# Optimization experiments

Hardware: AMD Instinct MI355X
Metric: run time of the kernel (lower is better)

## Reference

```python
import jax, jax.numpy as jnp
import numpy as np

SHAPES = ((28, 28, 28), (14, 14, 14), (7, 7, 7))  # (D,H,W) per level, hardcoded by offset_normalizer
M, L, P = 6, 3, 4  # n_heads, n_levels, n_points


def grid_sample_3d(vol, grid):
    """Trilinear grid sample, zeros padding, align_corners=False.
    vol: (B, C, D, H, W); grid: (B, Q, 3) with xyz in [-1,1] (x->W, y->H, z->D).
    Returns (B, C, Q)."""
    B, C, D, H, W = vol.shape
    x = ((grid[..., 0] + 1.0) * W - 1.0) * 0.5
    y = ((grid[..., 1] + 1.0) * H - 1.0) * 0.5
    z = ((grid[..., 2] + 1.0) * D - 1.0) * 0.5
    x0f = jnp.floor(x); y0f = jnp.floor(y); z0f = jnp.floor(z)
    fx = x - x0f; fy = y - y0f; fz = z - z0f
    x0 = x0f.astype(jnp.int32); y0 = y0f.astype(jnp.int32); z0 = z0f.astype(jnp.int32)
    flat = vol.reshape(B, C, D * H * W)
    out = jnp.zeros((B, C, grid.shape[1]), vol.dtype)
    for dz, wz in ((0, 1.0 - fz), (1, fz)):
        for dy, wy in ((0, 1.0 - fy), (1, fy)):
            for dx, wx in ((0, 1.0 - fx), (1, fx)):
                zi = z0 + dz; yi = y0 + dy; xi = x0 + dx
                valid = (zi >= 0) & (zi < D) & (yi >= 0) & (yi < H) & (xi >= 0) & (xi < W)
                idx = (jnp.clip(zi, 0, D - 1) * H + jnp.clip(yi, 0, H - 1)) * W + jnp.clip(xi, 0, W - 1)
                g = jnp.take_along_axis(flat, idx[:, None, :], axis=2)  # (B,C,Q)
                w = (wz * wy * wx) * valid.astype(vol.dtype)
                out = out + g * w[:, None, :]
    return out


def setup_inputs() -> dict:
    key = jax.random.key(0)
    ks = jax.random.split(key, 8)
    bs, Lq, d_model, image_dim, T = 1, 4096, 768, 1408, 2
    S = sum(d * h * w for d, h, w in SHAPES)  # 25039
    return {
        "query": jax.random.normal(ks[0], (bs, Lq, d_model), jnp.float32),
        "reference_points": jax.random.uniform(ks[1], (bs, Lq, 3), jnp.float32),
        "value": jax.random.normal(ks[2], (bs, T, S, image_dim), jnp.float32),
        "Wv": jax.random.normal(ks[3], (image_dim, d_model), jnp.float32) * 0.02,
        "bv": jnp.zeros((d_model,), jnp.float32),
        "Woff": jax.random.normal(ks[4], (d_model, M * T * L * P * 3), jnp.float32) * 0.02,
        "boff": jax.random.normal(ks[5], (M * T * L * P * 3,), jnp.float32) * 0.5,
        "Wa": jax.random.normal(ks[6], (d_model, M * T * L * P), jnp.float32) * 0.02,
        "ba": jnp.zeros((M * T * L * P,), jnp.float32),
        "Wo": jax.random.normal(ks[7], (d_model, d_model), jnp.float32) * 0.02,
        "bo": jnp.zeros((d_model,), jnp.float32),
    }


def reference(query, reference_points, value, Wv, bv, Woff, boff, Wa, ba, Wo, bo):
    N, Lq, d_model = query.shape
    T = value.shape[1]
    Dh = d_model // M
    # value projection + head split: (N,T,S,M,Dh)
    v = (value @ Wv + bv).reshape(N, T, -1, M, Dh)
    # sampling offsets and attention weights from query
    off = (query @ Woff + boff).reshape(N, Lq, M, T, L, P, 3)
    aw = jax.nn.softmax((query @ Wa + ba).reshape(N, Lq, M, T * L * P), axis=-1)
    aw = aw.reshape(N, Lq, M, T, L, P)
    normalizer = jnp.asarray([[28., 28., 28.], [14., 14., 14.], [7., 7., 7.]], query.dtype)
    loc = reference_points[:, :, None, None, None, None, :] + off / normalizer[None, None, None, None, :, None, :]
    grids = 2.0 * loc - 1.0  # (N,Lq,M,T,L,P,3)
    starts = [0]
    for (d, h, w) in SHAPES:
        starts.append(starts[-1] + d * h * w)
    sampled = []
    for l, (Dl, Hl, Wl) in enumerate(SHAPES):
        vl = v[:, :, starts[l]:starts[l + 1]]                       # (N,T,Sl,M,Dh)
        vl = vl.transpose(0, 1, 3, 4, 2).reshape(N * T * M, Dh, Dl, Hl, Wl)
        gl = grids[:, :, :, :, l].transpose(0, 3, 2, 1, 4, 5).reshape(N * T * M, Lq * P, 3)
        sampled.append(grid_sample_3d(vl, gl).reshape(N, T, M, Dh, Lq, P))
    s = jnp.stack(sampled, axis=5)                                  # (N,T,M,Dh,Lq,L,P)
    out = jnp.einsum('ntmdqlp,nqmtlp->nqmd', s, aw).reshape(N, Lq, M * Dh)
    return out @ Wo + bo
```

## Files before the change

### kernel.cpp

```cpp
#include <hip/hip_runtime.h>
#include <hip/hip_bf16.h>
#include <stdint.h>

#define LQ    4096
#define DMOD  768
#define IMGD  1408
#define TT    2
#define MM    6
#define LL    3
#define PP    4
#define DH    128
#define STOT  25039
#define OFFC  432
#define AWC   144
#define PROJC 576
#define NSAMP 24
#define NCORN 192

typedef __attribute__((ext_vector_type(8))) __bf16 bf16x8;
typedef __attribute__((ext_vector_type(4))) float  f32x4;

__device__ __forceinline__ void gl_lds16(const void* g, void* l) {
    __builtin_amdgcn_global_load_lds(
        (const __attribute__((address_space(1))) void*)g,
        (__attribute__((address_space(3))) void*)l, 16, 0, 0);
}

__global__ __launch_bounds__(256) void cvt_transpose(
    const float* __restrict__ W, __bf16* __restrict__ WT, int K, int N)
{
    __shared__ float tile[32][33];
    const int k0 = blockIdx.x * 32, n0 = blockIdx.y * 32;
    const int c = threadIdx.x & 31, r8 = threadIdx.x >> 5;
    #pragma unroll
    for (int i = 0; i < 4; ++i) {
        int r = r8 + i * 8;
        int k = k0 + r, n = n0 + c;
        tile[r][c] = (k < K && n < N) ? W[(size_t)k * N + n] : 0.f;
    }
    __syncthreads();
    #pragma unroll
    for (int i = 0; i < 4; ++i) {
        int r = r8 + i * 8;
        int n = n0 + r, k = k0 + c;
        if (n < N && k < K) WT[(size_t)n * K + k] = (__bf16)tile[c][r];
    }
}

__global__ __launch_bounds__(256) void cvt_value(
    const float4* __restrict__ src, __bf16* __restrict__ dst, int n4)
{
    int i = blockIdx.x * blockDim.x + threadIdx.x;
    const int stride = gridDim.x * blockDim.x;
    for (; i < n4; i += stride) {
        float4 v = src[i];
        union { __bf16 h[4]; uint64_t u; } pk;
        pk.h[0] = (__bf16)v.x; pk.h[1] = (__bf16)v.y;
        pk.h[2] = (__bf16)v.z; pk.h[3] = (__bf16)v.w;
        *(uint64_t*)(dst + (size_t)i * 4) = pk.u;
    }
}

__global__ void concat_bias(const float* __restrict__ boff,
                            const float* __restrict__ ba,
                            float* __restrict__ bcat)
{
    int i = blockIdx.x * blockDim.x + threadIdx.x;
    if (i < PROJC) bcat[i] = (i < OFFC) ? boff[i] : ba[i - OFFC];
}

template<bool A_BF16, bool OUT_BF16>
__global__ __launch_bounds__(256) void gemm_mfma(
    const void* __restrict__ Ap, const __bf16* __restrict__ BT,
    const float* __restrict__ bias, void* __restrict__ Cp,
    int M, int N, int K)
{
    __shared__ __bf16 As[128][32];
    __shared__ __bf16 Bs[128][32];

    const int tid  = threadIdx.x;
    const int lane = tid & 63;
    const int wave = tid >> 6;
    const int wm = (wave & 1) * 64;
    const int wn = (wave >> 1) * 64;
    const int row0 = blockIdx.y * 128;
    const int col0 = blockIdx.x * 128;
    const int fr = lane & 15;
    const int kq = lane >> 4;

    const int sr  = tid >> 1;
    const int kk0 = (tid & 1) * 16;

    f32x4 acc[4][4] = {};

    for (int kt = 0; kt < K; kt += 32) {
        #pragma unroll
        for (int j = 0; j < 2; ++j) {
            const int g   = wave * 128 + j * 64 + lane;
            const int row = g >> 2, cir = g & 3;
            const __bf16* src = BT + (size_t)(col0 + row) * K + kt + cir * 8;
            gl_lds16(src, (char*)&Bs[0][0] + (size_t)(wave * 128 + j * 64) * 16);
        }
        if constexpr (A_BF16) {
            const __bf16* A = (const __bf16*)Ap;
            #pragma unroll
            for (int j = 0; j < 2; ++j) {
                const int g   = wave * 128 + j * 64 + lane;
                const int row = g >> 2, cir = g & 3;
                const __bf16* src = A + (size_t)(row0 + row) * K + kt + cir * 8;
                gl_lds16(src, (char*)&As[0][0] + (size_t)(wave * 128 + j * 64) * 16);
            }
        } else {
            const float* A = (const float*)Ap;
            const int gm = row0 + sr;
            float f[16];
            if (gm < M) {
                const float4* ap = (const float4*)(A + (size_t)gm * K + kt + kk0);
                #pragma unroll
                for (int i = 0; i < 4; ++i) {
                    float4 v = ap[i];
                    f[i*4+0] = v.x; f[i*4+1] = v.y; f[i*4+2] = v.z; f[i*4+3] = v.w;
                }
            } else {
                #pragma unroll
                for (int i = 0; i < 16; ++i) f[i] = 0.f;
            }
            bf16x8 v0, v1;
            #pragma unroll
            for (int i = 0; i < 8; ++i) { v0[i] = (__bf16)f[i]; v1[i] = (__bf16)f[i+8]; }
            *(bf16x8*)&As[sr][kk0]     = v0;
            *(bf16x8*)&As[sr][kk0 + 8] = v1;
        }
        __syncthreads();

        bf16x8 a[4], b[4];
        #pragma unroll
        for (int mt = 0; mt < 4; ++mt) a[mt] = *(const bf16x8*)&As[wm + mt*16 + fr][kq * 8];
        #pragma unroll
        for (int nt = 0; nt < 4; ++nt) b[nt] = *(const bf16x8*)&Bs[wn + nt*16 + fr][kq * 8];
        #pragma unroll
        for (int mt = 0; mt < 4; ++mt)
            #pragma unroll
            for (int nt = 0; nt < 4; ++nt)
                acc[mt][nt] = __builtin_amdgcn_mfma_f32_16x16x32_bf16(
                    a[mt], b[nt], acc[mt][nt], 0, 0, 0);
        __syncthreads();
    }

    const int col = lane & 15;
    const int rq  = (lane >> 4) * 4;
    #pragma unroll
    for (int mt = 0; mt < 4; ++mt) {
        #pragma unroll
        for (int r = 0; r < 4; ++r) {
            const int gm = row0 + wm + mt*16 + rq + r;
            if (gm >= M) continue;
            #pragma unroll
            for (int nt = 0; nt < 4; ++nt) {
                const int gn = col0 + wn + nt*16 + col;
                if (gn < N) {
                    float v = acc[mt][nt][r] + bias[gn];
                    if constexpr (OUT_BF16)
                        ((__bf16*)Cp)[(size_t)gm * N + gn] = (__bf16)v;
                    else
                        ((float*)Cp)[(size_t)gm * N + gn] = v;
                }
            }
        }
    }
}

__global__ __launch_bounds__(256) void sample_kernel(
    const float* __restrict__ refp,
    const float* __restrict__ proj,
    const __bf16* __restrict__ vbuf,
    __bf16* __restrict__ attn)
{
    const int wave = threadIdx.x >> 6;
    const int lane = threadIdx.x & 63;
    const int q = blockIdx.x * 4 + wave;
    const int m = blockIdx.y;

    __shared__ float    s_aw[4][NSAMP];
    __shared__ float    s_w[4][NCORN];
    __shared__ uint32_t s_o[4][NCORN];

    if (lane < NSAMP)
        s_aw[wave][lane] = proj[(size_t)q * PROJC + OFFC + m * NSAMP + lane];
    __syncthreads();

    if (lane < NSAMP) {
        float mx = -1e30f;
        #pragma unroll
        for (int i = 0; i < NSAMP; ++i) mx = fmaxf(mx, s_aw[wave][i]);
        float sum = 0.f;
        #pragma unroll
        for (int i = 0; i < NSAMP; ++i) sum += __expf(s_aw[wave][i] - mx);
        const float aww = __expf(s_aw[wave][lane] - mx) / sum;

        const int t = lane / 12;
        const int r = lane - t * 12;
        const int l = r >> 2;
        const int   Dl    = (l == 0) ? 28 : (l == 1) ? 14 : 7;
        const int   start = (l == 0) ? 0  : (l == 1) ? 21952 : 24696;
        const float fD    = (float)Dl;
        const int   base  = t * STOT + start;

        const float* op = proj + (size_t)q * PROJC + m * 72 + lane * 3;
        const float rx = refp[q*3+0], ry = refp[q*3+1], rz = refp[q*3+2];
        float x = rx * fD + op[0] - 0.5f;
        float y = ry * fD + op[1] - 0.5f;
        float z = rz * fD + op[2] - 0.5f;
        float xf = floorf(x), yf = floorf(y), zf = floorf(z);
        float fx = x - xf, fy = y - yf, fz = z - zf;
        int x0 = (int)xf, y0 = (int)yf, z0 = (int)zf;
        float wx[2] = {1.f - fx, fx}, wy[2] = {1.f - fy, fy}, wz[2] = {1.f - fz, fz};
        #pragma unroll
        for (int cc = 0; cc < 8; ++cc) {
            int dx = cc & 1, dy = (cc >> 1) & 1, dz = cc >> 2;
            int xi = x0 + dx, yi = y0 + dy, zi = z0 + dz;
            bool ok = (xi >= 0) & (xi < Dl) & (yi >= 0) & (yi < Dl) &
                      (zi >= 0) & (zi < Dl);
            float    w   = ok ? aww * wx[dx] * wy[dy] * wz[dz] : 0.f;
            uint32_t off = ok ? (uint32_t)(base + (zi * Dl + yi) * Dl + xi) * (768u * 2u) : 0u;
            s_w[wave][lane * 8 + cc] = w;
            s_o[wave][lane * 8 + cc] = off;
        }
    }
    __syncthreads();

    const char* vb = (const char*)vbuf + ((size_t)m * 128 + lane * 2) * 2;
    float acc0 = 0.f, acc1 = 0.f;
    #pragma unroll 8
    for (int i = 0; i < NCORN; ++i) {
        const float    w   = s_w[wave][i];
        const uint32_t off = s_o[wave][i];
        const uint32_t u = *(const uint32_t*)(vb + off);
        acc0 += w * __uint_as_float(u << 16);
        acc1 += w * __uint_as_float(u & 0xffff0000u);
    }

    union { __bf16 h[2]; uint32_t u; } pk;
    pk.h[0] = (__bf16)acc0; pk.h[1] = (__bf16)acc1;
    *(uint32_t*)((char*)attn + ((size_t)q * DMOD + m * 128 + lane * 2) * 2) = pk.u;
}

extern "C" void kernel_launch(void* const* d_in, const int* in_sizes, int n_in,
                              void* d_out, int out_size, void* d_ws, size_t ws_size,
                              hipStream_t stream) {
    const float* query = (const float*)d_in[0];
    const float* refp  = (const float*)d_in[1];
    const float* value = (const float*)d_in[2];
    const float* Wv    = (const float*)d_in[3];
    const float* bv    = (const float*)d_in[4];
    const float* Woff  = (const float*)d_in[5];
    const float* boff  = (const float*)d_in[6];
    const float* Wa    = (const float*)d_in[7];
    const float* ba    = (const float*)d_in[8];
    const float* Wo    = (const float*)d_in[9];
    const float* bo    = (const float*)d_in[10];
    float* out = (float*)d_out;

    const size_t SZ_VALBF = (size_t)TT * STOT * IMGD * 2;
    const size_t SZ_VBUF  = (size_t)TT * STOT * DMOD * 2;
    const size_t SZ_PROJ  = (size_t)LQ * PROJC * 4;
    const size_t SZ_ATTN  = (size_t)LQ * DMOD * 2;
    const size_t SZ_WVT   = (size_t)IMGD * DMOD * 2;
    const size_t SZ_WCAT  = (size_t)PROJC * DMOD * 2;
    const size_t SZ_WOT   = (size_t)DMOD * DMOD * 2;
    const size_t NEED_FAST = SZ_VALBF + SZ_VBUF + SZ_PROJ + SZ_ATTN +
                             SZ_WVT + SZ_WCAT + SZ_WOT + 8192;
    const bool fast = ws_size >= NEED_FAST;

    char* p = (char*)d_ws;
    __bf16* valbf = nullptr;
    if (fast) { valbf = (__bf16*)p; p += SZ_VALBF; }
    __bf16* vbuf  = (__bf16*)p; p += SZ_VBUF;
    float*  proj  = (float*)p;  p += SZ_PROJ;
    __bf16* attn  = (__bf16*)p; p += SZ_ATTN;
    __bf16* wvt   = (__bf16*)p; p += SZ_WVT;
    __bf16* wcatT = (__bf16*)p; p += SZ_WCAT;
    __bf16* woT   = (__bf16*)p; p += SZ_WOT;
    float*  bcat  = (float*)p;

    cvt_transpose<<<dim3((IMGD+31)/32, (DMOD+31)/32), 256, 0, stream>>>(Wv, wvt, IMGD, DMOD);
    cvt_transpose<<<dim3((DMOD+31)/32, (OFFC+31)/32), 256, 0, stream>>>(Woff, wcatT, DMOD, OFFC);
    cvt_transpose<<<dim3((DMOD+31)/32, (AWC +31)/32), 256, 0, stream>>>(Wa, wcatT + (size_t)OFFC * DMOD, DMOD, AWC);
    cvt_transpose<<<dim3((DMOD+31)/32, (DMOD+31)/32), 256, 0, stream>>>(Wo, woT, DMOD, DMOD);
    concat_bias<<<dim3(3), 256, 0, stream>>>(boff, ba, bcat);

    const int Mv = TT * STOT;

    if (fast) {
        cvt_value<<<dim3(4096), 256, 0, stream>>>((const float4*)value, valbf,
                                                  (int)((size_t)TT * STOT * IMGD / 4));
        gemm_mfma<true, true><<<dim3(DMOD/128, (Mv+127)/128), 256, 0, stream>>>(
            valbf, wvt, bv, vbuf, Mv, DMOD, IMGD);
    } else {
        gemm_mfma<false, true><<<dim3(DMOD/128, (Mv+127)/128), 256, 0, stream>>>(
            value, wvt, bv, vbuf, Mv, DMOD, IMGD);
    }

    gemm_mfma<false, false><<<dim3((PROJC+127)/128, LQ/128), 256, 0, stream>>>(
        query, wcatT, bcat, proj, LQ, PROJC, DMOD);

    sample_kernel<<<dim3(LQ/4, MM), 256, 0, stream>>>(refp, proj, vbuf, attn);

    gemm_mfma<true, false><<<dim3(DMOD/128, LQ/128), 256, 0, stream>>>(
        attn, woT, bo, out, LQ, DMOD, DMOD);
}
```

Before: 766.1 us.

## Double-buffer GEMM, fuse value fp32 conversion, swizzle blocks per XCD, widen sampling loads

Drops the separate fp32-to-bf16 conversion pass over the value tensor. The value projection GEMM now reads fp32 directly and converts while staging into LDS. The GEMM gains double-buffered LDS with register prefetch of the next A tile, a single barrier per k-step, occupancy hint 3, and an XCD-aware block-index swizzle for the large value GEMM. The sampling kernel splits corners across wave halves, loads 8 bytes per lane and combines the halves with a cross-lane shuffle. This trades the extra conversion pass for more register pressure and fp32 global reads inside the GEMM.

```diff
diff --git a/kernel.cpp b/kernel.cpp
--- a/kernel.cpp
+++ b/kernel.cpp
@@ -47,20 +47,6 @@
     }
 }
 
-__global__ __launch_bounds__(256) void cvt_value(
-    const float4* __restrict__ src, __bf16* __restrict__ dst, int n4)
-{
-    int i = blockIdx.x * blockDim.x + threadIdx.x;
-    const int stride = gridDim.x * blockDim.x;
-    for (; i < n4; i += stride) {
-        float4 v = src[i];
-        union { __bf16 h[4]; uint64_t u; } pk;
-        pk.h[0] = (__bf16)v.x; pk.h[1] = (__bf16)v.y;
-        pk.h[2] = (__bf16)v.z; pk.h[3] = (__bf16)v.w;
-        *(uint64_t*)(dst + (size_t)i * 4) = pk.u;
-    }
-}
-
 __global__ void concat_bias(const float* __restrict__ boff,
                             const float* __restrict__ ba,
                             float* __restrict__ bcat)
@@ -69,82 +55,119 @@
     if (i < PROJC) bcat[i] = (i < OFFC) ? boff[i] : ba[i - OFFC];
 }
 
-template<bool A_BF16, bool OUT_BF16>
-__global__ __launch_bounds__(256) void gemm_mfma(
+template<int AF32, int OUT_BF16, int SWZ>
+__global__ __launch_bounds__(256, 3) void gemm_mfma(
     const void* __restrict__ Ap, const __bf16* __restrict__ BT,
     const float* __restrict__ bias, void* __restrict__ Cp,
     int M, int N, int K)
 {
-    __shared__ __bf16 As[128][32];
-    __shared__ __bf16 Bs[128][32];
+    __shared__ __bf16 As[2][128][32];
+    __shared__ __bf16 Bs[2][128][32];
 
     const int tid  = threadIdx.x;
     const int lane = tid & 63;
     const int wave = tid >> 6;
     const int wm = (wave & 1) * 64;
     const int wn = (wave >> 1) * 64;
-    const int row0 = blockIdx.y * 128;
-    const int col0 = blockIdx.x * 128;
+
+    int bx, by;
+    if constexpr (SWZ > 0) {
+        const int bid = blockIdx.x;
+        const int xcd = bid & 7;
+        const int slot = bid >> 3;
+        const int ppx = (gridDim.x >> 3) / SWZ;
+        const int pix = slot / SWZ;
+        bx = slot - pix * SWZ;
+        by = xcd * ppx + pix;
+    } else {
+        bx = blockIdx.x; by = blockIdx.y;
+    }
+    const int row0 = by * 128;
+    const int col0 = bx * 128;
+
     const int fr = lane & 15;
     const int kq = lane >> 4;
 
     const int sr  = tid >> 1;
     const int kk0 = (tid & 1) * 16;
-
-    f32x4 acc[4][4] = {};
-
-    for (int kt = 0; kt < K; kt += 32) {
+    const int gB_row = (wave * 128 + lane) >> 2;
+    (void)gB_row;
+
+    float f[16];
+
+    auto stageB = [&](int ki, int buf) {
         #pragma unroll
         for (int j = 0; j < 2; ++j) {
             const int g   = wave * 128 + j * 64 + lane;
             const int row = g >> 2, cir = g & 3;
-            const __bf16* src = BT + (size_t)(col0 + row) * K + kt + cir * 8;
-            gl_lds16(src, (char*)&Bs[0][0] + (size_t)(wave * 128 + j * 64) * 16);
-        }
-        if constexpr (A_BF16) {
-            const __bf16* A = (const __bf16*)Ap;
+            const __bf16* src = BT + (size_t)(col0 + row) * K + ki * 32 + cir * 8;
+            gl_lds16(src, (char*)&Bs[buf][0][0] + (size_t)(wave * 128 + j * 64) * 16);
+        }
+    };
+    auto stageA_lds = [&](int ki, int buf) {
+        const __bf16* A = (const __bf16*)Ap;
+        #pragma unroll
+        for (int j = 0; j < 2; ++j) {
+            const int g   = wave * 128 + j * 64 + lane;
+            const int row = g >> 2, cir = g & 3;
+            const __bf16* src = A + (size_t)(row0 + row) * K + ki * 32 + cir * 8;
+            gl_lds16(src, (char*)&As[buf][0][0] + (size_t)(wave * 128 + j * 64) * 16);
+        }
+    };
+    auto loadA_f32 = [&](int ki) {
+        const float* A = (const float*)Ap;
+        const int gm = row0 + sr;
+        if (gm < M) {
+            const float4* ap = (const float4*)(A + (size_t)gm * K + ki * 32 + kk0);
             #pragma unroll
-            for (int j = 0; j < 2; ++j) {
-                const int g   = wave * 128 + j * 64 + lane;
-                const int row = g >> 2, cir = g & 3;
-                const __bf16* src = A + (size_t)(row0 + row) * K + kt + cir * 8;
-                gl_lds16(src, (char*)&As[0][0] + (size_t)(wave * 128 + j * 64) * 16);
+            for (int i = 0; i < 4; ++i) {
+                float4 v = ap[i];
+                f[i*4+0] = v.x; f[i*4+1] = v.y; f[i*4+2] = v.z; f[i*4+3] = v.w;
             }
         } else {
-            const float* A = (const float*)Ap;
-            const int gm = row0 + sr;
-            float f[16];
-            if (gm < M) {
-                const float4* ap = (const float4*)(A + (size_t)gm * K + kt + kk0);
-                #pragma unroll
-                for (int i = 0; i < 4; ++i) {
-                    float4 v = ap[i];
-                    f[i*4+0] = v.x; f[i*4+1] = v.y; f[i*4+2] = v.z; f[i*4+3] = v.w;
-                }
-            } else {
-                #pragma unroll
-                for (int i = 0; i < 16; ++i) f[i] = 0.f;
-            }
-            bf16x8 v0, v1;
             #pragma unroll
-            for (int i = 0; i < 8; ++i) { v0[i] = (__bf16)f[i]; v1[i] = (__bf16)f[i+8]; }
-            *(bf16x8*)&As[sr][kk0]     = v0;
-            *(bf16x8*)&As[sr][kk0 + 8] = v1;
-        }
+            for (int i = 0; i < 16; ++i) f[i] = 0.f;
+        }
+    };
+    auto writeA = [&](int buf) {
+        bf16x8 v0, v1;
+        #pragma unroll
+        for (int i = 0; i < 8; ++i) { v0[i] = (__bf16)f[i]; v1[i] = (__bf16)f[i+8]; }
+        *(bf16x8*)&As[buf][sr][kk0]     = v0;
+        *(bf16x8*)&As[buf][sr][kk0 + 8] = v1;
+    };
+
+    f32x4 acc[4][4] = {};
+    const int nk = K >> 5;
+
+    stageB(0, 0);
+    if constexpr (AF32) { loadA_f32(0); writeA(0); }
+    else                { stageA_lds(0, 0); }
+
+    for (int i = 0; i < nk; ++i) {
         __syncthreads();
+        const int cur = i & 1, nxt = cur ^ 1;
+        const bool more = (i + 1) < nk;
+
+        if (more) {
+            stageB(i + 1, nxt);
+            if constexpr (AF32) loadA_f32(i + 1);
+            else                stageA_lds(i + 1, nxt);
+        }
 
         bf16x8 a[4], b[4];
         #pragma unroll
-        for (int mt = 0; mt < 4; ++mt) a[mt] = *(const bf16x8*)&As[wm + mt*16 + fr][kq * 8];
-        #pragma unroll
-        for (int nt = 0; nt < 4; ++nt) b[nt] = *(const bf16x8*)&Bs[wn + nt*16 + fr][kq * 8];
+        for (int mt = 0; mt < 4; ++mt) a[mt] = *(const bf16x8*)&As[cur][wm + mt*16 + fr][kq * 8];
+        #pragma unroll
+        for (int nt = 0; nt < 4; ++nt) b[nt] = *(const bf16x8*)&Bs[cur][wn + nt*16 + fr][kq * 8];
         #pragma unroll
         for (int mt = 0; mt < 4; ++mt)
             #pragma unroll
             for (int nt = 0; nt < 4; ++nt)
                 acc[mt][nt] = __builtin_amdgcn_mfma_f32_16x16x32_bf16(
                     a[mt], b[nt], acc[mt][nt], 0, 0, 0);
-        __syncthreads();
+
+        if constexpr (AF32) { if (more) writeA(nxt); }
     }
 
     const int col = lane & 15;
@@ -229,20 +252,31 @@
     }
     __syncthreads();
 
-    const char* vb = (const char*)vbuf + ((size_t)m * 128 + lane * 2) * 2;
-    float acc0 = 0.f, acc1 = 0.f;
-    #pragma unroll 8
-    for (int i = 0; i < NCORN; ++i) {
-        const float    w   = s_w[wave][i];
-        const uint32_t off = s_o[wave][i];
-        const uint32_t u = *(const uint32_t*)(vb + off);
-        acc0 += w * __uint_as_float(u << 16);
-        acc1 += w * __uint_as_float(u & 0xffff0000u);
-    }
-
-    union { __bf16 h[2]; uint32_t u; } pk;
-    pk.h[0] = (__bf16)acc0; pk.h[1] = (__bf16)acc1;
-    *(uint32_t*)((char*)attn + ((size_t)q * DMOD + m * 128 + lane * 2) * 2) = pk.u;
+    const int h = lane >> 5;
+    const int c = lane & 31;
+    const char* vb = (const char*)vbuf + ((size_t)m * 128 + c * 4) * 2;
+    float a0 = 0.f, a1 = 0.f, a2 = 0.f, a3 = 0.f;
+    #pragma unroll 4
+    for (int i = 0; i < NCORN / 2; ++i) {
+        const float    w   = s_w[wave][2 * i + h];
+        const uint32_t off = s_o[wave][2 * i + h];
+        const uint2 u = *(const uint2*)(vb + off);
+        a0 += w * __uint_as_float(u.x << 16);
+        a1 += w * __uint_as_float(u.x & 0xffff0000u);
+        a2 += w * __uint_as_float(u.y << 16);
+        a3 += w * __uint_as_float(u.y & 0xffff0000u);
+    }
+    a0 += __shfl_xor(a0, 32);
+    a1 += __shfl_xor(a1, 32);
+    a2 += __shfl_xor(a2, 32);
+    a3 += __shfl_xor(a3, 32);
+
+    if (h == 0) {
+        union { __bf16 hh[4]; uint2 u; } pk;
+        pk.hh[0] = (__bf16)a0; pk.hh[1] = (__bf16)a1;
+        pk.hh[2] = (__bf16)a2; pk.hh[3] = (__bf16)a3;
+        *(uint2*)((char*)attn + ((size_t)q * DMOD + m * 128 + c * 4) * 2) = pk.u;
+    }
 }
 
 extern "C" void kernel_launch(void* const* d_in, const int* in_sizes, int n_in,
@@ -261,20 +295,14 @@
     const float* bo    = (const float*)d_in[10];
     float* out = (float*)d_out;
 
-    const size_t SZ_VALBF = (size_t)TT * STOT * IMGD * 2;
-    const size_t SZ_VBUF  = (size_t)TT * STOT * DMOD * 2;
-    const size_t SZ_PROJ  = (size_t)LQ * PROJC * 4;
-    const size_t SZ_ATTN  = (size_t)LQ * DMOD * 2;
-    const size_t SZ_WVT   = (size_t)IMGD * DMOD * 2;
-    const size_t SZ_WCAT  = (size_t)PROJC * DMOD * 2;
-    const size_t SZ_WOT   = (size_t)DMOD * DMOD * 2;
-    const size_t NEED_FAST = SZ_VALBF + SZ_VBUF + SZ_PROJ + SZ_ATTN +
-                             SZ_WVT + SZ_WCAT + SZ_WOT + 8192;
-    const bool fast = ws_size >= NEED_FAST;
+    const size_t SZ_VBUF = (size_t)TT * STOT * DMOD * 2;
+    const size_t SZ_PROJ = (size_t)LQ * PROJC * 4;
+    const size_t SZ_ATTN = (size_t)LQ * DMOD * 2;
+    const size_t SZ_WVT  = (size_t)IMGD * DMOD * 2;
+    const size_t SZ_WCAT = (size_t)PROJC * DMOD * 2;
+    const size_t SZ_WOT  = (size_t)DMOD * DMOD * 2;
 
     char* p = (char*)d_ws;
-    __bf16* valbf = nullptr;
-    if (fast) { valbf = (__bf16*)p; p += SZ_VALBF; }
     __bf16* vbuf  = (__bf16*)p; p += SZ_VBUF;
     float*  proj  = (float*)p;  p += SZ_PROJ;
     __bf16* attn  = (__bf16*)p; p += SZ_ATTN;
@@ -291,21 +319,14 @@
 
     const int Mv = TT * STOT;
 
-    if (fast) {
-        cvt_value<<<dim3(4096), 256, 0, stream>>>((const float4*)value, valbf,
-                                                  (int)((size_t)TT * STOT * IMGD / 4));
-        gemm_mfma<true, true><<<dim3(DMOD/128, (Mv+127)/128), 256, 0, stream>>>(
-            valbf, wvt, bv, vbuf, Mv, DMOD, IMGD);
-    } else {
-        gemm_mfma<false, true><<<dim3(DMOD/128, (Mv+127)/128), 256, 0, stream>>>(
-            value, wvt, bv, vbuf, Mv, DMOD, IMGD);
-    }
-
-    gemm_mfma<false, false><<<dim3((PROJC+127)/128, LQ/128), 256, 0, stream>>>(
+    gemm_mfma<1, 1, 6><<<dim3(2352), 256, 0, stream>>>(
+        value, wvt, bv, vbuf, Mv, DMOD, IMGD);
+
+    gemm_mfma<1, 0, 0><<<dim3((PROJC + 127) / 128, LQ / 128), 256, 0, stream>>>(
         query, wcatT, bcat, proj, LQ, PROJC, DMOD);
 
-    sample_kernel<<<dim3(LQ/4, MM), 256, 0, stream>>>(refp, proj, vbuf, attn);
-
-    gemm_mfma<true, false><<<dim3(DMOD/128, LQ/128), 256, 0, stream>>>(
+    sample_kernel<<<dim3(LQ / 4, MM), 256, 0, stream>>>(refp, proj, vbuf, attn);
+
+    gemm_mfma<0, 0, 0><<<dim3(DMOD / 128, LQ / 128), 256, 0, stream>>>(
         attn, woT, bo, out, LQ, DMOD, DMOD);
 }
```

New measurement: 731.7 us. 4.5% less time.
